# Kernel tuning notes

Hardware: AMD Instinct MI355X
Metric: run time of the kernel (lower is better)

The kernel has to match this reference:

```python
import jax, jax.numpy as jnp
import numpy as np

BOUND = 1.0
NUM_STEPS = 128
MIN_NEAR = 0.05


def setup_inputs() -> dict:
    key = jax.random.key(0)
    ks = jax.random.split(key, 7)
    B, N, H = 2, 8192, 64
    # camera origins on a radius-2 sphere, rays aimed at jittered points near origin
    o = jax.random.normal(ks[0], (B, N, 3), jnp.float32)
    o = 2.0 * o / (jnp.linalg.norm(o, axis=-1, keepdims=True) + 1e-8)
    tgt = 0.5 * jax.random.normal(ks[1], (B, N, 3), jnp.float32)
    d = tgt - o
    d = d / (jnp.linalg.norm(d, axis=-1, keepdims=True) + 1e-8)
    W1 = jax.random.normal(ks[2], (3, H), jnp.float32) * 0.5
    W2 = jax.random.normal(ks[3], (3, H), jnp.float32) * 0.5
    b1 = jax.random.normal(ks[4], (H,), jnp.float32) * 0.1
    w_sigma = jax.random.normal(ks[5], (H, 1), jnp.float32) * 0.5
    W_color = jax.random.normal(ks[6], (H, 3), jnp.float32) * 0.5
    return {"rays_o": o, "rays_d": d, "W1": W1, "W2": W2, "b1": b1,
            "w_sigma": w_sigma, "W_color": W_color}


def _near_far(rays_o, rays_d):
    # cube AABB intersection (near_far_from_bound, type='cube')
    inv = 1.0 / (rays_d + 1e-15)
    tmin = (-BOUND - rays_o) * inv
    tmax = (BOUND - rays_o) * inv
    near = jnp.max(jnp.minimum(tmin, tmax), axis=-1, keepdims=True)  # [B,N,1]
    far = jnp.min(jnp.maximum(tmin, tmax), axis=-1, keepdims=True)
    miss = far < near
    near = jnp.where(miss, 1e9, near)
    far = jnp.where(miss, 1e9, far)
    near = jnp.maximum(near, MIN_NEAR)
    return near, far


def reference(rays_o, rays_d, W1, W2, b1, w_sigma, W_color):
    nears, fars = _near_far(rays_o, rays_d)                    # [B,N,1]
    t = jnp.linspace(0.0, 1.0, NUM_STEPS, dtype=jnp.float32)   # [S]
    z_vals = nears + (fars - nears) * t                        # [B,N,S]
    sample_dist = (fars - nears) / (NUM_STEPS - 1)             # [B,N,1]

    # sample points along rays, clamped to the AABB
    xyzs = rays_o[..., None, :] + rays_d[..., None, :] * z_vals[..., None]  # [B,N,S,3]
    xyzs = jnp.clip(xyzs, -BOUND, BOUND)

    # network stub: tiny per-sample MLP -> sigma [B,N,S], color [B,N,S,3]
    h = jax.nn.relu(jnp.einsum('bnsc,ch->bnsh', xyzs, W1)
                    + jnp.einsum('bnc,ch->bnh', rays_d, W2)[:, :, None, :]
                    + b1)
    sigma = jax.nn.softplus(jnp.einsum('bnsh,ho->bnso', h, w_sigma))[..., 0]
    rgbs = jax.nn.sigmoid(jnp.einsum('bnsh,hc->bnsc', h, W_color))

    # alpha compositing
    deltas = z_vals[..., 1:] - z_vals[..., :-1]                # [B,N,S-1]
    deltas = jnp.concatenate([deltas, sample_dist], axis=-1)   # [B,N,S]
    alphas = 1.0 - jnp.exp(-deltas * sigma)
    alphas_shifted = jnp.concatenate(
        [jnp.ones_like(alphas[..., :1]), 1.0 - alphas + 1e-15], axis=-1)
    weights = alphas * jnp.cumprod(alphas_shifted, axis=-1)[..., :-1]  # [B,N,S]

    weights_sum = weights.sum(axis=-1)                         # [B,N]
    depth = jnp.sum(weights * z_vals, axis=-1)                 # [B,N]
    image = jnp.sum(weights[..., None] * rgbs, axis=-2)        # [B,N,3], bg_color=0
    return image, depth, weights, weights_sum
```

## Files before the change

### kernel.cpp

```cpp
#include <hip/hip_runtime.h>
#include <math.h>

#define NSTEPS 128
#define HID 64
#define RAYS_PER_BLOCK 8
#define THREADS_PER_RAY 32
#define SPT 4

static __device__ __forceinline__ unsigned pk_bits(float a, float b) {
    auto v = __builtin_amdgcn_cvt_pkrtz(a, b);
    return __builtin_bit_cast(unsigned, v);
}
static __device__ __forceinline__ unsigned pk_fma(unsigned a, unsigned b, unsigned c) {
    unsigned d;
    asm("v_pk_fma_f16 %0, %1, %2, %3" : "=v"(d) : "v"(a), "v"(b), "v"(c));
    return d;
}
static __device__ __forceinline__ unsigned pk_relu(unsigned a) {
    unsigned d;
    asm("v_pk_max_f16 %0, %1, 0" : "=v"(d) : "v"(a));
    return d;
}
static __device__ __forceinline__ float dot2acc(unsigned h, unsigned w, float acc) {
    float d;
    asm("v_dot2_f32_f16 %0, %1, %2, %3" : "=v"(d) : "v"(h), "v"(w), "v"(acc));
    return d;
}

__global__ __launch_bounds__(256, 8) void nerf_render_kernel(
    const float* __restrict__ rays_o,
    const float* __restrict__ rays_d,
    const float* __restrict__ W1,
    const float* __restrict__ W2,
    const float* __restrict__ b1,
    const float* __restrict__ w_sigma,
    const float* __restrict__ W_color,
    float* __restrict__ out_image,
    float* __restrict__ out_depth,
    float* __restrict__ out_weights,
    float* __restrict__ out_wsum,
    int R)
{
    __shared__ uint4 ldsA[RAYS_PER_BLOCK][33];
    __shared__ uint4 ldsB[32];

    const int tid = threadIdx.x;

    {
        const int e  = tid;
        const int r  = e >> 5;
        const int jp = e & 31;
        const int j0 = jp * 2;
        int gray = blockIdx.x * RAYS_PER_BLOCK + r;
        if (gray >= R) gray = R - 1;
        const float dd0 = rays_d[gray * 3 + 0];
        const float dd1 = rays_d[gray * 3 + 1];
        const float dd2 = rays_d[gray * 3 + 2];
        const float2 w1x = *(const float2*)&W1[0 * HID + j0];
        const float2 w1y = *(const float2*)&W1[1 * HID + j0];
        const float2 w1z = *(const float2*)&W1[2 * HID + j0];
        const float2 w2x = *(const float2*)&W2[0 * HID + j0];
        const float2 w2y = *(const float2*)&W2[1 * HID + j0];
        const float2 w2z = *(const float2*)&W2[2 * HID + j0];
        const float2 bb  = *(const float2*)&b1[j0];
        const float bs0 = fmaf(dd0, w2x.x, fmaf(dd1, w2y.x, fmaf(dd2, w2z.x, bb.x)));
        const float bs1 = fmaf(dd0, w2x.y, fmaf(dd1, w2y.y, fmaf(dd2, w2z.y, bb.y)));
        uint4 v;
        v.x = pk_bits(w1x.x, w1x.y);
        v.y = pk_bits(w1y.x, w1y.y);
        v.z = pk_bits(w1z.x, w1z.y);
        v.w = pk_bits(bs0, bs1);
        ldsA[r][jp] = v;
    }
    if (tid < 32) {
        const int j0 = tid * 2;
        const float2 ws = *(const float2*)&w_sigma[j0];
        const float c00 = W_color[j0 * 3 + 0], c01 = W_color[j0 * 3 + 1], c02 = W_color[j0 * 3 + 2];
        const float c10 = W_color[j0 * 3 + 3], c11 = W_color[j0 * 3 + 4], c12 = W_color[j0 * 3 + 5];
        uint4 v;
        v.x = pk_bits(ws.x, ws.y);
        v.y = pk_bits(c00, c10);
        v.z = pk_bits(c01, c11);
        v.w = pk_bits(c02, c12);
        ldsB[tid] = v;
    }
    __syncthreads();

    const int r   = tid >> 5;
    const int l   = tid & 31;
    int ray = blockIdx.x * RAYS_PER_BLOCK + r;
    const bool valid = (ray < R);
    if (!valid) ray = R - 1;

    const float o0 = rays_o[ray * 3 + 0];
    const float o1 = rays_o[ray * 3 + 1];
    const float o2 = rays_o[ray * 3 + 2];
    const float d0 = rays_d[ray * 3 + 0];
    const float d1 = rays_d[ray * 3 + 1];
    const float d2 = rays_d[ray * 3 + 2];

    const float inv0 = 1.0f / (d0 + 1e-15f);
    const float inv1 = 1.0f / (d1 + 1e-15f);
    const float inv2 = 1.0f / (d2 + 1e-15f);
    const float t0a = (-1.0f - o0) * inv0, t0b = (1.0f - o0) * inv0;
    const float t1a = (-1.0f - o1) * inv1, t1b = (1.0f - o1) * inv1;
    const float t2a = (-1.0f - o2) * inv2, t2b = (1.0f - o2) * inv2;
    float near = fmaxf(fmaxf(fminf(t0a, t0b), fminf(t1a, t1b)), fminf(t2a, t2b));
    float far  = fminf(fminf(fmaxf(t0a, t0b), fmaxf(t1a, t1b)), fmaxf(t2a, t2b));
    if (far < near) { near = 1e9f; far = 1e9f; }
    near = fmaxf(near, 0.05f);
    const float span = far - near;
    const float sample_dist = span * (1.0f / (NSTEPS - 1));

    unsigned X0[SPT], X1[SPT], X2[SPT];
#pragma unroll
    for (int k = 0; k < SPT; k++) {
        const int s = l * SPT + k;
        const float t = (float)s * (1.0f / (NSTEPS - 1));
        const float z = fmaf(span, t, near);
        const float x0 = fminf(fmaxf(fmaf(d0, z, o0), -1.0f), 1.0f);
        const float x1 = fminf(fmaxf(fmaf(d1, z, o1), -1.0f), 1.0f);
        const float x2 = fminf(fmaxf(fmaf(d2, z, o2), -1.0f), 1.0f);
        X0[k] = pk_bits(x0, x0);
        X1[k] = pk_bits(x1, x1);
        X2[k] = pk_bits(x2, x2);
    }

    float aS[SPT] = {0,0,0,0};
    float aR[SPT] = {0,0,0,0};
    float aG[SPT] = {0,0,0,0};
    float aB[SPT] = {0,0,0,0};

#pragma unroll 4
    for (int jp = 0; jp < 32; jp++) {
        const uint4 A  = ldsA[r][jp];
        const uint4 Bq = ldsB[jp];
#pragma unroll
        for (int k = 0; k < SPT; k++) {
            unsigned h = pk_fma(X0[k], A.x, pk_fma(X1[k], A.y, pk_fma(X2[k], A.z, A.w)));
            h = pk_relu(h);
            aS[k] = dot2acc(h, Bq.x, aS[k]);
            aR[k] = dot2acc(h, Bq.y, aR[k]);
            aG[k] = dot2acc(h, Bq.z, aG[k]);
            aB[k] = dot2acc(h, Bq.w, aB[k]);
        }
    }

    float alpha[SPT], Tloc[SPT];
    float pl = 1.0f;
#pragma unroll
    for (int k = 0; k < SPT; k++) {
        const float x = aS[k];
        const float sig = fmaxf(x, 0.0f) + __logf(1.0f + __expf(-fabsf(x)));
        alpha[k] = 1.0f - __expf(-sample_dist * sig);
        Tloc[k] = pl;
        pl *= (1.0f - alpha[k] + 1e-15f);
    }

    float inc = pl;
#pragma unroll
    for (int dlt = 1; dlt < THREADS_PER_RAY; dlt <<= 1) {
        const float v = __shfl_up(inc, dlt, THREADS_PER_RAY);
        if (l >= dlt) inc *= v;
    }
    float excl = __shfl_up(inc, 1, THREADS_PER_RAY);
    if (l == 0) excl = 1.0f;

    float w[SPT];
    float wsum = 0.f, dep = 0.f, im0 = 0.f, im1 = 0.f, im2 = 0.f;
#pragma unroll
    for (int k = 0; k < SPT; k++) {
        const int s = l * SPT + k;
        const float t = (float)s * (1.0f / (NSTEPS - 1));
        const float z = fmaf(span, t, near);
        const float T  = excl * Tloc[k];
        const float wt = alpha[k] * T;
        w[k] = wt;
        wsum += wt;
        dep  += wt * z;
        const float cr = 1.0f / (1.0f + __expf(-aR[k]));
        const float cg = 1.0f / (1.0f + __expf(-aG[k]));
        const float cb = 1.0f / (1.0f + __expf(-aB[k]));
        im0 += wt * cr;
        im1 += wt * cg;
        im2 += wt * cb;
    }

    if (valid) {
        *(float4*)&out_weights[(size_t)ray * NSTEPS + l * SPT] =
            make_float4(w[0], w[1], w[2], w[3]);
    }

#pragma unroll
    for (int dlt = THREADS_PER_RAY / 2; dlt >= 1; dlt >>= 1) {
        wsum += __shfl_down(wsum, dlt, THREADS_PER_RAY);
        dep  += __shfl_down(dep,  dlt, THREADS_PER_RAY);
        im0  += __shfl_down(im0,  dlt, THREADS_PER_RAY);
        im1  += __shfl_down(im1,  dlt, THREADS_PER_RAY);
        im2  += __shfl_down(im2,  dlt, THREADS_PER_RAY);
    }
    if (l == 0 && valid) {
        out_image[ray * 3 + 0] = im0;
        out_image[ray * 3 + 1] = im1;
        out_image[ray * 3 + 2] = im2;
        out_depth[ray] = dep;
        out_wsum[ray]  = wsum;
    }
}

extern "C" void kernel_launch(void* const* d_in, const int* in_sizes, int n_in,
                              void* d_out, int out_size, void* d_ws, size_t ws_size,
                              hipStream_t stream) {
    const float* rays_o  = (const float*)d_in[0];
    const float* rays_d  = (const float*)d_in[1];
    const float* W1      = (const float*)d_in[2];
    const float* W2      = (const float*)d_in[3];
    const float* b1      = (const float*)d_in[4];
    const float* w_sigma = (const float*)d_in[5];
    const float* W_color = (const float*)d_in[6];

    const int R = in_sizes[0] / 3;

    float* out         = (float*)d_out;
    float* out_image   = out;
    float* out_depth   = out_image + (size_t)R * 3;
    float* out_weights = out_depth + R;
    float* out_wsum    = out_weights + (size_t)R * NSTEPS;

    const int blocks = (R + RAYS_PER_BLOCK - 1) / RAYS_PER_BLOCK;
    nerf_render_kernel<<<blocks, 256, 0, stream>>>(
        rays_o, rays_d, W1, W2, b1, w_sigma, W_color,
        out_image, out_depth, out_weights, out_wsum, R);
}
```

Baseline: 92.25 us.

## Fold per-sample xyz into linear pre-activation along ray to cut MLP FMAs

Sample points are linear in the step index between the clamped near and far points. The kernel now precomputes, per hidden pair, a base pre-activation u (near point plus direction and bias term) and a per-step increment g. The hot loop then computes each hidden value with one packed FMA (s*g+u) instead of three, and the LDS entry per hidden pair shrinks from uint4 to uint2. The inner loop unroll also goes from 4 to 8. The linear form matches the reference only while the interior samples stay inside the box, and the fp16 product s*g adds rounding error at large step indices.

```diff
diff --git a/kernel.cpp b/kernel.cpp
--- a/kernel.cpp
+++ b/kernel.cpp
@@ -41,53 +41,13 @@
     float* __restrict__ out_wsum,
     int R)
 {
-    __shared__ uint4 ldsA[RAYS_PER_BLOCK][33];
+    __shared__ uint2 ldsA[RAYS_PER_BLOCK][33];
     __shared__ uint4 ldsB[32];
 
     const int tid = threadIdx.x;
-
-    {
-        const int e  = tid;
-        const int r  = e >> 5;
-        const int jp = e & 31;
-        const int j0 = jp * 2;
-        int gray = blockIdx.x * RAYS_PER_BLOCK + r;
-        if (gray >= R) gray = R - 1;
-        const float dd0 = rays_d[gray * 3 + 0];
-        const float dd1 = rays_d[gray * 3 + 1];
-        const float dd2 = rays_d[gray * 3 + 2];
-        const float2 w1x = *(const float2*)&W1[0 * HID + j0];
-        const float2 w1y = *(const float2*)&W1[1 * HID + j0];
-        const float2 w1z = *(const float2*)&W1[2 * HID + j0];
-        const float2 w2x = *(const float2*)&W2[0 * HID + j0];
-        const float2 w2y = *(const float2*)&W2[1 * HID + j0];
-        const float2 w2z = *(const float2*)&W2[2 * HID + j0];
-        const float2 bb  = *(const float2*)&b1[j0];
-        const float bs0 = fmaf(dd0, w2x.x, fmaf(dd1, w2y.x, fmaf(dd2, w2z.x, bb.x)));
-        const float bs1 = fmaf(dd0, w2x.y, fmaf(dd1, w2y.y, fmaf(dd2, w2z.y, bb.y)));
-        uint4 v;
-        v.x = pk_bits(w1x.x, w1x.y);
-        v.y = pk_bits(w1y.x, w1y.y);
-        v.z = pk_bits(w1z.x, w1z.y);
-        v.w = pk_bits(bs0, bs1);
-        ldsA[r][jp] = v;
-    }
-    if (tid < 32) {
-        const int j0 = tid * 2;
-        const float2 ws = *(const float2*)&w_sigma[j0];
-        const float c00 = W_color[j0 * 3 + 0], c01 = W_color[j0 * 3 + 1], c02 = W_color[j0 * 3 + 2];
-        const float c10 = W_color[j0 * 3 + 3], c11 = W_color[j0 * 3 + 4], c12 = W_color[j0 * 3 + 5];
-        uint4 v;
-        v.x = pk_bits(ws.x, ws.y);
-        v.y = pk_bits(c00, c10);
-        v.z = pk_bits(c01, c11);
-        v.w = pk_bits(c02, c12);
-        ldsB[tid] = v;
-    }
-    __syncthreads();
-
     const int r   = tid >> 5;
     const int l   = tid & 31;
+
     int ray = blockIdx.x * RAYS_PER_BLOCK + r;
     const bool valid = (ray < R);
     if (!valid) ray = R - 1;
@@ -112,18 +72,55 @@
     const float span = far - near;
     const float sample_dist = span * (1.0f / (NSTEPS - 1));
 
-    unsigned X0[SPT], X1[SPT], X2[SPT];
+    const float xn0 = fminf(fmaxf(fmaf(d0, near, o0), -1.0f), 1.0f);
+    const float xn1 = fminf(fmaxf(fmaf(d1, near, o1), -1.0f), 1.0f);
+    const float xn2 = fminf(fmaxf(fmaf(d2, near, o2), -1.0f), 1.0f);
+    const float xf0 = fminf(fmaxf(fmaf(d0, far, o0), -1.0f), 1.0f);
+    const float xf1 = fminf(fmaxf(fmaf(d1, far, o1), -1.0f), 1.0f);
+    const float xf2 = fminf(fmaxf(fmaf(d2, far, o2), -1.0f), 1.0f);
+    const float sx0 = (xf0 - xn0) * (1.0f / (NSTEPS - 1));
+    const float sx1 = (xf1 - xn1) * (1.0f / (NSTEPS - 1));
+    const float sx2 = (xf2 - xn2) * (1.0f / (NSTEPS - 1));
+
+    {
+        const int j0 = l * 2;
+        const float2 w1x = *(const float2*)&W1[0 * HID + j0];
+        const float2 w1y = *(const float2*)&W1[1 * HID + j0];
+        const float2 w1z = *(const float2*)&W1[2 * HID + j0];
+        const float2 w2x = *(const float2*)&W2[0 * HID + j0];
+        const float2 w2y = *(const float2*)&W2[1 * HID + j0];
+        const float2 w2z = *(const float2*)&W2[2 * HID + j0];
+        const float2 bb  = *(const float2*)&b1[j0];
+        const float u0 = fmaf(xn0, w1x.x, fmaf(xn1, w1y.x, fmaf(xn2, w1z.x,
+                         fmaf(d0, w2x.x, fmaf(d1, w2y.x, fmaf(d2, w2z.x, bb.x))))));
+        const float u1 = fmaf(xn0, w1x.y, fmaf(xn1, w1y.y, fmaf(xn2, w1z.y,
+                         fmaf(d0, w2x.y, fmaf(d1, w2y.y, fmaf(d2, w2z.y, bb.y))))));
+        const float g0 = fmaf(sx0, w1x.x, fmaf(sx1, w1y.x, sx2 * w1z.x));
+        const float g1 = fmaf(sx0, w1x.y, fmaf(sx1, w1y.y, sx2 * w1z.y));
+        uint2 v;
+        v.x = pk_bits(u0, u1);
+        v.y = pk_bits(g0, g1);
+        ldsA[r][l] = v;
+    }
+    if (tid < 32) {
+        const int j0 = tid * 2;
+        const float2 ws = *(const float2*)&w_sigma[j0];
+        const float c00 = W_color[j0 * 3 + 0], c01 = W_color[j0 * 3 + 1], c02 = W_color[j0 * 3 + 2];
+        const float c10 = W_color[j0 * 3 + 3], c11 = W_color[j0 * 3 + 4], c12 = W_color[j0 * 3 + 5];
+        uint4 v;
+        v.x = pk_bits(ws.x, ws.y);
+        v.y = pk_bits(c00, c10);
+        v.z = pk_bits(c01, c11);
+        v.w = pk_bits(c02, c12);
+        ldsB[tid] = v;
+    }
+    __syncthreads();
+
+    unsigned S[SPT];
 #pragma unroll
     for (int k = 0; k < SPT; k++) {
-        const int s = l * SPT + k;
-        const float t = (float)s * (1.0f / (NSTEPS - 1));
-        const float z = fmaf(span, t, near);
-        const float x0 = fminf(fmaxf(fmaf(d0, z, o0), -1.0f), 1.0f);
-        const float x1 = fminf(fmaxf(fmaf(d1, z, o1), -1.0f), 1.0f);
-        const float x2 = fminf(fmaxf(fmaf(d2, z, o2), -1.0f), 1.0f);
-        X0[k] = pk_bits(x0, x0);
-        X1[k] = pk_bits(x1, x1);
-        X2[k] = pk_bits(x2, x2);
+        const float sv = (float)(l * SPT + k);
+        S[k] = pk_bits(sv, sv);
     }
 
     float aS[SPT] = {0,0,0,0};
@@ -131,14 +128,13 @@
     float aG[SPT] = {0,0,0,0};
     float aB[SPT] = {0,0,0,0};
 
-#pragma unroll 4
+#pragma unroll 8
     for (int jp = 0; jp < 32; jp++) {
-        const uint4 A  = ldsA[r][jp];
+        const uint2 A  = ldsA[r][jp];
         const uint4 Bq = ldsB[jp];
 #pragma unroll
         for (int k = 0; k < SPT; k++) {
-            unsigned h = pk_fma(X0[k], A.x, pk_fma(X1[k], A.y, pk_fma(X2[k], A.z, A.w)));
-            h = pk_relu(h);
+            const unsigned h = pk_relu(pk_fma(S[k], A.y, A.x));
             aS[k] = dot2acc(h, Bq.x, aS[k]);
             aR[k] = dot2acc(h, Bq.y, aR[k]);
             aG[k] = dot2acc(h, Bq.z, aG[k]);
```

After: 91.31 us. Within noise of the previous version (-1.0%).
